# Kernel optimization log

Hardware: AMD Instinct MI355X
Metric: run time of the kernel (lower is better)

Reference implementation:

```python
import jax, jax.numpy as jnp
import numpy as np

B, S, D = 4, 2048, 1024
D_K, D_V = 1024, 1024


def setup_inputs() -> dict:
    key = jax.random.key(0)
    ks = jax.random.split(key, 9)
    s = 1.0 / np.sqrt(D)
    return {
        "q_in": jax.random.normal(ks[0], (B, S, D), jnp.float32),
        "k_in": jax.random.normal(ks[1], (B, S, D), jnp.float32),
        "v_in": jax.random.normal(ks[2], (B, S, D), jnp.float32),
        "Wq": jax.random.normal(ks[3], (D, D_K), jnp.float32) * s,
        "bq": jnp.zeros((D_K,), jnp.float32),
        "Wk": jax.random.normal(ks[4], (D, D_K), jnp.float32) * s,
        "bk": jnp.zeros((D_K,), jnp.float32),
        "Wv": jax.random.normal(ks[5], (D, D_V), jnp.float32) * s,
        "bv": jnp.zeros((D_V,), jnp.float32),
    }


def reference(q_in, k_in, v_in, Wq, bq, Wk, bk, Wv, bv):
    q = jnp.einsum("bsd,dk->bsk", q_in, Wq) + bq  # [B,S,d_k]
    k = jnp.einsum("bsd,dk->bsk", k_in, Wk) + bk  # [B,S,d_k]
    v = jnp.einsum("bsd,dv->bsv", v_in, Wv) + bv  # [B,S,d_v]
    scores = jnp.einsum("bqk,bsk->bqs", q, k) / jnp.sqrt(jnp.float32(D_K))
    attn = jax.nn.softmax(scores, axis=-1)  # [B,S,S]
    return jnp.einsum("bqs,bsv->bqv", attn, v)
```

## Files before the change

### kernel.cpp

```cpp
#include <hip/hip_runtime.h>
#include <stdint.h>

#define B_  4
#define S_  2048
#define D_  1024
#define DK_ 1024
#define DV_ 1024

typedef __attribute__((ext_vector_type(8)))  short short8;
typedef __attribute__((ext_vector_type(16))) float floatx16;

#define ASYNC16(gsrc, ldst)                                                        \
  __builtin_amdgcn_global_load_lds(                                                \
      (const __attribute__((address_space(1))) unsigned int*)(gsrc),               \
      (__attribute__((address_space(3))) unsigned int*)(ldst), 16, 0, 0)

#define WAITVM(N) asm volatile("s_waitcnt vmcnt(" #N ")" ::: "memory")

__device__ __forceinline__ unsigned short f2bf(float f) {
  union { float f; uint32_t u; } v; v.f = f;
  uint32_t r = v.u + 0x7fffu + ((v.u >> 16) & 1u);
  return (unsigned short)(r >> 16);
}

__global__ __launch_bounds__(256)
void prep(const float* __restrict__ q, const float* __restrict__ k, const float* __restrict__ v,
          const float* __restrict__ W0, const float* __restrict__ W1, const float* __restrict__ W2,
          unsigned short* __restrict__ qkv, unsigned short* __restrict__ WT) {
  const int bid = blockIdx.x, tid = threadIdx.x;
  if (bid < 12288) {
    const int t  = bid >> 12;
    const int cb = bid & 4095;
    const float* in = (t == 0) ? q : (t == 1) ? k : v;
    unsigned short* o = qkv + (long)t * ((long)B_ * S_ * D_);
    const int i0 = cb * 512 + tid;
    float4 v0 = ((const float4*)in)[i0];
    float4 v1 = ((const float4*)in)[i0 + 256];
    ushort4 u0, u1;
    u0.x = f2bf(v0.x); u0.y = f2bf(v0.y); u0.z = f2bf(v0.z); u0.w = f2bf(v0.w);
    u1.x = f2bf(v1.x); u1.y = f2bf(v1.y); u1.z = f2bf(v1.z); u1.w = f2bf(v1.w);
    ((ushort4*)o)[i0] = u0;
    ((ushort4*)o)[i0 + 256] = u1;
  } else {
    const int b2 = bid - 12288;
    const int w  = b2 >> 10;
    const int tl = b2 & 1023;
    const float* in = (w == 0) ? W0 : (w == 1) ? W1 : W2;
    unsigned short* o = WT + (long)w * D_ * DK_;
    __shared__ float tile[32][33];
    const int bx = (tl & 31) * 32, by = (tl >> 5) * 32;
    const int tx = tid & 31, ty = tid >> 5;
    for (int r = ty; r < 32; r += 8)
      tile[r][tx] = in[(long)(by + r) * DK_ + bx + tx];
    __syncthreads();
    for (int r = ty; r < 32; r += 8)
      o[(long)(bx + r) * D_ + by + tx] = f2bf(tile[tx][r]);
  }
}

__device__ __forceinline__ void storeC(float* p, float v)          { *p = v; }
__device__ __forceinline__ void storeC(unsigned short* p, float v) { *p = f2bf(v); }

template <typename OutT, int NOUT, int MODE>
__global__ __launch_bounds__(256)
void gemm_bt32(const unsigned short* __restrict__ A0, const unsigned short* __restrict__ A1,
               const unsigned short* __restrict__ A2, const unsigned short* __restrict__ Bm,
               OutT* __restrict__ C0, OutT* __restrict__ C1, OutT* __restrict__ C2,
               const float* __restrict__ b0, const float* __restrict__ b1,
               const float* __restrict__ b2, float* __restrict__ rowsum,
               int N, int K, long sA, long sB, long sC, float scale) {
  __shared__ __align__(16) unsigned short As[3][128 * 32];
  __shared__ __align__(16) unsigned short Bs[3][128 * 32];
  __shared__ float invs[128];
  const int tid  = threadIdx.x;
  const int lane = tid & 63, wave = tid >> 6;
  const int wm = (wave >> 1) * 64, wn = (wave & 1) * 64;
  const int lm = lane & 31;
  const int hi = lane >> 5;

  const int gx = gridDim.x, gy = gridDim.y;
  const int T  = gx * gy * (int)gridDim.z;
  const int l  = blockIdx.x + gx * (blockIdx.y + gy * blockIdx.z);
  const int l2 = (l & 7) * (T >> 3) + (l >> 3);
  const int bxi = l2 % gx;
  const int byi = (l2 / gx) % gy;
  const int bzi = l2 / (gx * gy);

  const long zb = bzi;
  const int m0  = byi * 128;
  const int n0g = bxi * 128;

  const unsigned short* A = A0;
  OutT* C = C0;
  const float* bias = b0;
  int n0 = n0g, sel = 0;
  if (NOUT == 3) {
    sel = n0g >> 10;
    n0 = n0g & 1023;
    if (sel == 1)      { A = A1; C = C1; bias = b1; }
    else if (sel == 2) { A = A2; C = C2; bias = b2; }
  }
  A += zb * sA;
  const unsigned short* Bp = Bm + zb * sB;
  C += zb * sC;

  const int rr = lane >> 2;
  const int cc = (((lane & 3) ^ ((lane >> 3) & 3)) * 8);
  const unsigned short* gA0 = A  + (long)(m0  + 16 * wave + rr) * K + cc;
  const unsigned short* gA1 = gA0 + 64 * (long)K;
  const unsigned short* gB0 = Bp + (long)(n0g + 16 * wave + rr) * K + cc;
  const unsigned short* gB1 = gB0 + 64 * (long)K;
  const int la0 = wave * 512, la1 = (wave + 4) * 512;

  floatx16 acc[2][2] = {};
  const int sw = (lm >> 1) & 3;

#define GEMM_COMPUTE(pp)                                                                \
  _Pragma("unroll")                                                                     \
  for (int s = 0; s < 2; s++) {                                                         \
    const int off = ((s * 2 + hi) ^ sw) * 8;                                            \
    short8 af[2], bf[2];                                                                \
    _Pragma("unroll")                                                                   \
    for (int i = 0; i < 2; i++)                                                         \
      af[i] = *(const short8*)&As[pp][(wm + i * 32 + lm) * 32 + off];                   \
    _Pragma("unroll")                                                                   \
    for (int j = 0; j < 2; j++)                                                         \
      bf[j] = *(const short8*)&Bs[pp][(wn + j * 32 + lm) * 32 + off];                   \
    _Pragma("unroll")                                                                   \
    for (int i = 0; i < 2; i++)                                                         \
      _Pragma("unroll")                                                                 \
      for (int j = 0; j < 2; j++)                                                       \
        acc[i][j] = __builtin_amdgcn_mfma_f32_32x32x16_bf16(af[i], bf[j], acc[i][j], 0, 0, 0); \
  }

  ASYNC16(gA0, &As[0][la0]); ASYNC16(gA1, &As[0][la1]);
  ASYNC16(gB0, &Bs[0][la0]); ASYNC16(gB1, &Bs[0][la1]);
  gA0 += 32; gA1 += 32; gB0 += 32; gB1 += 32;
  ASYNC16(gA0, &As[1][la0]); ASYNC16(gA1, &As[1][la1]);
  ASYNC16(gB0, &Bs[1][la0]); ASYNC16(gB1, &Bs[1][la1]);
  gA0 += 32; gA1 += 32; gB0 += 32; gB1 += 32;

  const int nk = K >> 5;
  int pc = 0, pn = 2;
  for (int kt = 0; kt < nk - 1; kt++) {
    WAITVM(4);
    __builtin_amdgcn_s_barrier();
    if (kt + 2 < nk) {
      ASYNC16(gA0, &As[pn][la0]); ASYNC16(gA1, &As[pn][la1]);
      ASYNC16(gB0, &Bs[pn][la0]); ASYNC16(gB1, &Bs[pn][la1]);
      gA0 += 32; gA1 += 32; gB0 += 32; gB1 += 32;
    }
    GEMM_COMPUTE(pc)
    pc = (pc == 2) ? 0 : pc + 1;
    pn = (pn == 2) ? 0 : pn + 1;
  }
  WAITVM(0);
  __builtin_amdgcn_s_barrier();
  GEMM_COMPUTE(pc)

  if (MODE == 2) {
    __syncthreads();
    if (tid < 128) invs[tid] = 1.0f / rowsum[zb * S_ + m0 + tid];
    __syncthreads();
  }

  if (NOUT == 3 && sel == 2) {
    unsigned short* Vt = (unsigned short*)C;
    const int b = m0 >> 11;
    const int sbase = (m0 & 2047);
#pragma unroll
    for (int i = 0; i < 2; i++) {
      const int srowb = sbase + wm + i * 32 + (hi << 2);
#pragma unroll
      for (int j = 0; j < 2; j++) {
        const int col = n0 + wn + j * 32 + lm;
        const float bv = bias[col];
        unsigned short* vp = Vt + ((long)b * DV_ + col) * S_ + srowb;
#pragma unroll
        for (int g = 0; g < 4; g++) {
          ushort4 u;
          u.x = f2bf(acc[i][j][4 * g + 0] + bv);
          u.y = f2bf(acc[i][j][4 * g + 1] + bv);
          u.z = f2bf(acc[i][j][4 * g + 2] + bv);
          u.w = f2bf(acc[i][j][4 * g + 3] + bv);
          *(ushort4*)(vp + 8 * g) = u;
        }
      }
    }
  } else if (MODE == 1) {
#pragma unroll
    for (int i = 0; i < 2; i++) {
#pragma unroll
      for (int r = 0; r < 16; r++) {
        const int row = m0 + wm + i * 32 + (r & 3) + ((r >> 2) << 3) + (hi << 2);
        float sum2 = 0.f;
#pragma unroll
        for (int j = 0; j < 2; j++) {
          const int col = n0 + wn + j * 32 + lm;
          float e = __expf(acc[i][j][r] * scale);
          storeC(C + (long)row * N + col, e);
          sum2 += e;
        }
#pragma unroll
        for (int msk = 1; msk < 32; msk <<= 1) sum2 += __shfl_xor(sum2, msk, 64);
        if ((lane & 31) == 0) atomicAdd(&rowsum[zb * S_ + row], sum2);
      }
    }
  } else {
#pragma unroll
    for (int i = 0; i < 2; i++) {
#pragma unroll
      for (int j = 0; j < 2; j++) {
        const int col = n0 + wn + j * 32 + lm;
        const float bv = bias ? bias[col] : 0.f;
#pragma unroll
        for (int r = 0; r < 16; r++) {
          const int rl = wm + i * 32 + (r & 3) + ((r >> 2) << 3) + (hi << 2);
          float val = acc[i][j][r] * scale + bv;
          if (MODE == 2) val *= invs[rl];
          storeC(C + (long)(m0 + rl) * N + col, val);
        }
      }
    }
  }
#undef GEMM_COMPUTE
}

extern "C" void kernel_launch(void* const* d_in, const int* in_sizes, int n_in,
                              void* d_out, int out_size, void* d_ws, size_t ws_size,
                              hipStream_t stream) {
  const float* q_in = (const float*)d_in[0];
  const float* k_in = (const float*)d_in[1];
  const float* v_in = (const float*)d_in[2];
  const float* Wq   = (const float*)d_in[3];
  const float* bq   = (const float*)d_in[4];
  const float* Wk   = (const float*)d_in[5];
  const float* bk   = (const float*)d_in[6];
  const float* Wv   = (const float*)d_in[7];
  const float* bv   = (const float*)d_in[8];
  float* out = (float*)d_out;

  char* ws = (char*)d_ws;
  const long nX = (long)B_ * S_ * D_;
  const long nW = (long)D_ * DK_;
  unsigned short* qb  = (unsigned short*)(ws);
  unsigned short* kb  = qb + nX;
  unsigned short* vb  = kb + nX;
  unsigned short* WqT = vb + nX;
  unsigned short* Qb  = WqT + 3 * nW;
  unsigned short* Kb  = Qb + nX;
  unsigned short* Vt  = Kb + nX;
  float*          rowsum = (float*)(Vt + nX);
  unsigned short* U   = (unsigned short*)ws;

  dim3 blk(256);

  hipMemsetAsync(rowsum, 0, (size_t)B_ * S_ * sizeof(float), stream);

  {
    dim3 g(12288 + 3072);
    prep<<<g, blk, 0, stream>>>(q_in, k_in, v_in, Wq, Wk, Wv, qb, WqT);
  }
  {
    dim3 g(3 * DK_ / 128, (B_ * S_) / 128, 1);
    gemm_bt32<unsigned short, 3, 0><<<g, blk, 0, stream>>>(
        qb, kb, vb, WqT, Qb, Kb, Vt, bq, bk, bv, nullptr, DK_, D_, 0, 0, 0, 1.f);
  }
  {
    dim3 g(S_ / 128, S_ / 128, B_);
    gemm_bt32<unsigned short, 1, 1><<<g, blk, 0, stream>>>(
        Qb, nullptr, nullptr, Kb, U, nullptr, nullptr, nullptr, nullptr, nullptr, rowsum,
        S_, DK_, (long)S_ * DK_, (long)S_ * DK_, (long)S_ * S_, 0.03125f);
  }
  {
    dim3 g(DV_ / 128, S_ / 128, B_);
    gemm_bt32<float, 1, 2><<<g, blk, 0, stream>>>(
        U, nullptr, nullptr, Vt, out, nullptr, nullptr, nullptr, nullptr, nullptr, rowsum,
        DV_, S_, (long)S_ * S_, (long)DV_ * S_, (long)S_ * DV_, 1.f);
  }
}
```

Before: 352.5 us.

## Grow GEMM tiles to 256x256 with 8 waves and split-K the final PV GEMM

Doubles the block tile from 128x128 to 256x256 using 512-thread blocks, where each wave computes a 128x64 sub-tile, to raise arithmetic intensity and reuse per LDS load. Because the larger tiles leave the final attention-times-V GEMM with too few blocks, it is split along K into two halves. The halves accumulate into the zeroed output via float atomicAdd. This adds a memset of the output, atomic traffic, and doubles LDS use per block, which may limit occupancy. Smaller grids for the other GEMMs may also underfill the CUs.

```diff
diff --git a/kernel.cpp b/kernel.cpp
--- a/kernel.cpp
+++ b/kernel.cpp
@@ -61,20 +61,21 @@
 __device__ __forceinline__ void storeC(float* p, float v)          { *p = v; }
 __device__ __forceinline__ void storeC(unsigned short* p, float v) { *p = f2bf(v); }
 
-template <typename OutT, int NOUT, int MODE>
-__global__ __launch_bounds__(256)
-void gemm_bt32(const unsigned short* __restrict__ A0, const unsigned short* __restrict__ A1,
-               const unsigned short* __restrict__ A2, const unsigned short* __restrict__ Bm,
-               OutT* __restrict__ C0, OutT* __restrict__ C1, OutT* __restrict__ C2,
-               const float* __restrict__ b0, const float* __restrict__ b1,
-               const float* __restrict__ b2, float* __restrict__ rowsum,
-               int N, int K, long sA, long sB, long sC, float scale) {
-  __shared__ __align__(16) unsigned short As[3][128 * 32];
-  __shared__ __align__(16) unsigned short Bs[3][128 * 32];
-  __shared__ float invs[128];
+template <typename OutT, int NOUT, int MODE, int KSPL>
+__global__ __launch_bounds__(512, 2)
+void gemm_bt256(const unsigned short* __restrict__ A0, const unsigned short* __restrict__ A1,
+                const unsigned short* __restrict__ A2, const unsigned short* __restrict__ Bm,
+                OutT* __restrict__ C0, OutT* __restrict__ C1, OutT* __restrict__ C2,
+                const float* __restrict__ b0, const float* __restrict__ b1,
+                const float* __restrict__ b2, float* __restrict__ rowsum,
+                int N, int K, int lda, int ldb, long sA, long sB, long sC, float scale) {
+  __shared__ __align__(16) unsigned short As[3][256 * 32];
+  __shared__ __align__(16) unsigned short Bs[3][256 * 32];
+  __shared__ float invs[256];
   const int tid  = threadIdx.x;
   const int lane = tid & 63, wave = tid >> 6;
-  const int wm = (wave >> 1) * 64, wn = (wave & 1) * 64;
+  const int wm = (wave >> 2) * 128;
+  const int wn = (wave & 3) * 64;
   const int lm = lane & 31;
   const int hi = lane >> 5;
 
@@ -86,9 +87,10 @@
   const int byi = (l2 / gx) % gy;
   const int bzi = l2 / (gx * gy);
 
-  const long zb = bzi;
-  const int m0  = byi * 128;
-  const int n0g = bxi * 128;
+  const int  kh = (KSPL > 1) ? (bzi & (KSPL - 1)) : 0;
+  const long zb = (KSPL > 1) ? (bzi >> 1) : bzi;
+  const int m0  = byi * 256;
+  const int n0g = bxi * 256;
 
   const unsigned short* A = A0;
   OutT* C = C0;
@@ -100,34 +102,34 @@
     if (sel == 1)      { A = A1; C = C1; bias = b1; }
     else if (sel == 2) { A = A2; C = C2; bias = b2; }
   }
-  A += zb * sA;
-  const unsigned short* Bp = Bm + zb * sB;
+  A += zb * sA + (long)kh * K;
+  const unsigned short* Bp = Bm + zb * sB + (long)kh * K;
   C += zb * sC;
 
   const int rr = lane >> 2;
   const int cc = (((lane & 3) ^ ((lane >> 3) & 3)) * 8);
-  const unsigned short* gA0 = A  + (long)(m0  + 16 * wave + rr) * K + cc;
-  const unsigned short* gA1 = gA0 + 64 * (long)K;
-  const unsigned short* gB0 = Bp + (long)(n0g + 16 * wave + rr) * K + cc;
-  const unsigned short* gB1 = gB0 + 64 * (long)K;
-  const int la0 = wave * 512, la1 = (wave + 4) * 512;
-
-  floatx16 acc[2][2] = {};
+  const unsigned short* gA0 = A  + (long)(m0  + 16 * wave + rr) * lda + cc;
+  const unsigned short* gA1 = gA0 + 128 * (long)lda;
+  const unsigned short* gB0 = Bp + (long)(n0g + 16 * wave + rr) * ldb + cc;
+  const unsigned short* gB1 = gB0 + 128 * (long)ldb;
+  const int la0 = wave * 512, la1 = (wave + 8) * 512;
+
+  floatx16 acc[4][2] = {};
   const int sw = (lm >> 1) & 3;
 
 #define GEMM_COMPUTE(pp)                                                                \
   _Pragma("unroll")                                                                     \
   for (int s = 0; s < 2; s++) {                                                         \
     const int off = ((s * 2 + hi) ^ sw) * 8;                                            \
-    short8 af[2], bf[2];                                                                \
+    short8 af[4], bf[2];                                                                \
     _Pragma("unroll")                                                                   \
-    for (int i = 0; i < 2; i++)                                                         \
+    for (int i = 0; i < 4; i++)                                                         \
       af[i] = *(const short8*)&As[pp][(wm + i * 32 + lm) * 32 + off];                   \
     _Pragma("unroll")                                                                   \
     for (int j = 0; j < 2; j++)                                                         \
       bf[j] = *(const short8*)&Bs[pp][(wn + j * 32 + lm) * 32 + off];                   \
     _Pragma("unroll")                                                                   \
-    for (int i = 0; i < 2; i++)                                                         \
+    for (int i = 0; i < 4; i++)                                                         \
       _Pragma("unroll")                                                                 \
       for (int j = 0; j < 2; j++)                                                       \
         acc[i][j] = __builtin_amdgcn_mfma_f32_32x32x16_bf16(af[i], bf[j], acc[i][j], 0, 0, 0); \
@@ -158,9 +160,9 @@
   __builtin_amdgcn_s_barrier();
   GEMM_COMPUTE(pc)
 
-  if (MODE == 2) {
+  if (MODE == 2 || MODE == 3) {
     __syncthreads();
-    if (tid < 128) invs[tid] = 1.0f / rowsum[zb * S_ + m0 + tid];
+    if (tid < 256) invs[tid] = 1.0f / rowsum[zb * S_ + m0 + tid];
     __syncthreads();
   }
 
@@ -169,7 +171,7 @@
     const int b = m0 >> 11;
     const int sbase = (m0 & 2047);
 #pragma unroll
-    for (int i = 0; i < 2; i++) {
+    for (int i = 0; i < 4; i++) {
       const int srowb = sbase + wm + i * 32 + (hi << 2);
 #pragma unroll
       for (int j = 0; j < 2; j++) {
@@ -189,7 +191,7 @@
     }
   } else if (MODE == 1) {
 #pragma unroll
-    for (int i = 0; i < 2; i++) {
+    for (int i = 0; i < 4; i++) {
 #pragma unroll
       for (int r = 0; r < 16; r++) {
         const int row = m0 + wm + i * 32 + (r & 3) + ((r >> 2) << 3) + (hi << 2);
@@ -208,7 +210,7 @@
     }
   } else {
 #pragma unroll
-    for (int i = 0; i < 2; i++) {
+    for (int i = 0; i < 4; i++) {
 #pragma unroll
       for (int j = 0; j < 2; j++) {
         const int col = n0 + wn + j * 32 + lm;
@@ -217,8 +219,12 @@
         for (int r = 0; r < 16; r++) {
           const int rl = wm + i * 32 + (r & 3) + ((r >> 2) << 3) + (hi << 2);
           float val = acc[i][j][r] * scale + bv;
-          if (MODE == 2) val *= invs[rl];
-          storeC(C + (long)(m0 + rl) * N + col, val);
+          if (MODE == 3) {
+            atomicAdd((float*)(C + (long)(m0 + rl) * N + col), val * invs[rl]);
+          } else {
+            if (MODE == 2) val *= invs[rl];
+            storeC(C + (long)(m0 + rl) * N + col, val);
+          }
         }
       }
     }
@@ -253,29 +259,31 @@
   float*          rowsum = (float*)(Vt + nX);
   unsigned short* U   = (unsigned short*)ws;
 
-  dim3 blk(256);
+  dim3 blk(256), blk5(512);
 
   hipMemsetAsync(rowsum, 0, (size_t)B_ * S_ * sizeof(float), stream);
+  hipMemsetAsync(out, 0, (size_t)B_ * S_ * DV_ * sizeof(float), stream);
 
   {
     dim3 g(12288 + 3072);
     prep<<<g, blk, 0, stream>>>(q_in, k_in, v_in, Wq, Wk, Wv, qb, WqT);
   }
   {
-    dim3 g(3 * DK_ / 128, (B_ * S_) / 128, 1);
-    gemm_bt32<unsigned short, 3, 0><<<g, blk, 0, stream>>>(
-        qb, kb, vb, WqT, Qb, Kb, Vt, bq, bk, bv, nullptr, DK_, D_, 0, 0, 0, 1.f);
-  }
-  {
-    dim3 g(S_ / 128, S_ / 128, B_);
-    gemm_bt32<unsigned short, 1, 1><<<g, blk, 0, stream>>>(
+    dim3 g(3 * DK_ / 256, (B_ * S_) / 256, 1);
+    gemm_bt256<unsigned short, 3, 0, 1><<<g, blk5, 0, stream>>>(
+        qb, kb, vb, WqT, Qb, Kb, Vt, bq, bk, bv, nullptr,
+        DK_, D_, D_, D_, 0, 0, 0, 1.f);
+  }
+  {
+    dim3 g(S_ / 256, S_ / 256, B_);
+    gemm_bt256<unsigned short, 1, 1, 1><<<g, blk5, 0, stream>>>(
         Qb, nullptr, nullptr, Kb, U, nullptr, nullptr, nullptr, nullptr, nullptr, rowsum,
-        S_, DK_, (long)S_ * DK_, (long)S_ * DK_, (long)S_ * S_, 0.03125f);
-  }
-  {
-    dim3 g(DV_ / 128, S_ / 128, B_);
-    gemm_bt32<float, 1, 2><<<g, blk, 0, stream>>>(
+        S_, DK_, DK_, DK_, (long)S_ * DK_, (long)S_ * DK_, (long)S_ * S_, 0.03125f);
+  }
+  {
+    dim3 g(DV_ / 256, S_ / 256, B_ * 2);
+    gemm_bt256<float, 1, 3, 2><<<g, blk5, 0, stream>>>(
         U, nullptr, nullptr, Vt, out, nullptr, nullptr, nullptr, nullptr, nullptr, rowsum,
-        DV_, S_, (long)S_ * S_, (long)DV_ * S_, (long)S_ * DV_, 1.f);
-  }
-}
+        DV_, S_ / 2, S_, S_, (long)S_ * S_, (long)DV_ * S_, (long)S_ * DV_, 1.f);
+  }
+}
```

Measured after the change: 390.2 us. +10.7%, slower.
